# Performance work log

Measured on AMD Instinct MI355X. Metric: run time of the kernel, lower is better.

The kernel has to match this reference:

```python
import jax, jax.numpy as jnp
import numpy as np

EDGES = np.array([[0,6],[0,5],[6,8],[5,7],[0,62],[62,63],[63,64],[59,64],[59,60],[60,61],[61,62],[0,74],[71,72],[72,73],[73,74],[74,75],[75,76],[76,77],[77,78],[78,79],[79,80],[80,81],[81,82],[71,82],[71,83],[77,87],[83,84],[84,85],[85,86],[86,87],[87,88],[88,89],[89,90],[83,90],[0,65],[65,66],[66,67],[67,68],[68,69],[69,70],[65,70],[7,91],[91,92],[92,93],[93,94],[94,95],[91,96],[96,97],[97,98],[98,99],[91,100],[100,101],[101,102],[102,103],[91,104],[104,105],[105,106],[106,107],[91,108],[108,109],[109,110],[110,111],[8,112],[112,113],[113,114],[114,115],[115,116],[112,117],[117,118],[118,119],[119,120],[112,121],[121,122],[122,123],[123,124],[112,125],[125,126],[126,127],[127,128],[112,129],[129,130],[130,131],[131,132]], dtype=np.int32)
N_NODES = 102


def _gcn_structure():
    # Keep only edges whose endpoints fit in the 102-node feature view,
    # add self-loops, and compute symmetric GCN normalization (PyG gcn_norm).
    keep = (EDGES[:, 0] < N_NODES) & (EDGES[:, 1] < N_NODES)
    e = EDGES[keep]
    row, col = e[:, 0], e[:, 1]
    loops = np.arange(N_NODES, dtype=np.int32)
    row_f = np.concatenate([row, loops])
    col_f = np.concatenate([col, loops])
    deg = np.zeros(N_NODES, dtype=np.float32)
    np.add.at(deg, col_f, 1.0)  # in-degree incl. self-loop
    dinv = 1.0 / np.sqrt(np.maximum(deg, 1.0))
    norm = (dinv[row_f] * dinv[col_f]).astype(np.float32)
    return row_f, col_f, norm

_ROW, _COL, _NORM = _gcn_structure()


def setup_inputs() -> dict:
    key = jax.random.key(0)
    ks = jax.random.split(key, 5)
    B = 8192
    return {
        "x": jax.random.normal(ks[0], (B, 204), dtype=jnp.float32),
        "W_gcn": jax.random.normal(ks[1], (2, 64), dtype=jnp.float32) * 0.5,
        "b_gcn": jax.random.normal(ks[2], (64,), dtype=jnp.float32) * 0.1,
        "W_proj": jax.random.normal(ks[3], (64, 128), dtype=jnp.float32) * 0.1,
        "b_proj": jax.random.normal(ks[4], (128,), dtype=jnp.float32) * 0.1,
    }


def reference(x, W_gcn, b_gcn, W_proj, b_proj):
    B = x.shape[0]
    xn = x.reshape(B, N_NODES, 2)                      # (B, 102, 2)
    h = jnp.einsum('bni,ih->bnh', xn, W_gcn)           # GCN linear: (B, 102, H)
    norm = jnp.asarray(_NORM)
    msgs = h[:, _ROW, :] * norm[None, :, None]         # gather + normalize: (B, E+N, H)
    agg = jnp.zeros_like(h).at[:, _COL, :].add(msgs)   # scatter-add into targets
    agg = agg + b_gcn                                  # GCN bias
    act = jax.nn.relu(agg)                             # activation
    out = jnp.einsum('bnh,he->bne', act, W_proj) + b_proj  # projection: (B, 102, 128)
    return out
```

## Files before the change

### kernel.cpp

```cpp
#include <hip/hip_runtime.h>
#include <hip/hip_bf16.h>

#define NN   102
#define NE   83
#define NPAD 128

using bf16x8 = __attribute__((ext_vector_type(8))) short;
using f32x4  = __attribute__((ext_vector_type(4))) float;

__device__ __constant__ int EDGES_C[NE * 2] = {
    0,6, 0,5, 6,8, 5,7, 0,62, 62,63, 63,64, 59,64, 59,60, 60,61, 61,62,
    0,74, 71,72, 72,73, 73,74, 74,75, 75,76, 76,77, 77,78, 78,79, 79,80,
    80,81, 81,82, 71,82, 71,83, 77,87, 83,84, 84,85, 85,86, 86,87, 87,88,
    88,89, 89,90, 83,90, 0,65, 65,66, 66,67, 67,68, 68,69, 69,70, 65,70,
    7,91, 91,92, 92,93, 93,94, 94,95, 91,96, 96,97, 97,98, 98,99, 91,100,
    100,101, 101,102, 102,103, 91,104, 104,105, 105,106, 106,107, 91,108,
    108,109, 109,110, 110,111, 8,112, 112,113, 113,114, 114,115, 115,116,
    112,117, 117,118, 118,119, 119,120, 112,121, 121,122, 122,123, 123,124,
    112,125, 125,126, 126,127, 127,128, 112,129, 129,130, 130,131, 131,132
};

#define WS_BFRAG 0
#define WS_OFF   16384
#define WS_ER    (16384 + 512)
#define WS_EN    (16384 + 512 + 1024)

__device__ inline unsigned short f2bf(float f) {
  union { float f; unsigned u; } v; v.f = f;
  unsigned r = v.u + 0x7fffu + ((v.u >> 16) & 1u);
  return (unsigned short)(r >> 16);
}

__device__ inline unsigned cvt_pk_bf16(float lo, float hi) {
  unsigned r;
  asm("v_cvt_pk_bf16_f32 %0, %1, %2" : "=v"(r) : "v"(lo), "v"(hi));
  return r;
}

__global__ void gnn_setup(const float* __restrict__ Wp, char* __restrict__ ws) {
  const int t = threadIdx.x;

  if (blockIdx.x != 0) {
    unsigned short* bf = (unsigned short*)(ws + WS_BFRAG);
    for (int idx = t; idx < 16 * 64; idx += 256) {
      int lane = idx & 63;
      int f    = idx >> 6;
      int mt   = f >> 1, kc = f & 1;
      int e    = mt * 16 + (lane & 15);
      int kb   = kc * 32 + (lane >> 4) * 8;
      unsigned short* dst = bf + idx * 8;
#pragma unroll
      for (int i = 0; i < 8; ++i) dst[i] = f2bf(Wp[(kb + i) * 128 + e]);
    }
    return;
  }

  __shared__ float s_dinv[NN];
  __shared__ int   s_cnt[NN];
  __shared__ int   s_off[NN + 1];

  if (t < NN) {
    int deg = 1, cnt = 1;
    for (int e = 0; e < NE; ++e) {
      int r = EDGES_C[2*e], c = EDGES_C[2*e+1];
      if (r < NN && c == t) { ++deg; ++cnt; }
    }
    s_dinv[t] = 1.0f / sqrtf((float)deg);
    s_cnt[t]  = cnt;
  }
  __syncthreads();
  if (t < NN) {
    int o = 0;
    for (int c = 0; c < t; ++c) o += s_cnt[c];
    s_off[t] = o;
    if (t == NN - 1) s_off[NN] = o + s_cnt[t];
  }
  __syncthreads();
  int*   off = (int*)(ws + WS_OFF);
  int*   er  = (int*)(ws + WS_ER);
  float* en  = (float*)(ws + WS_EN);
  if (t < NN) {
    int c = t, pos = s_off[c];
    float dc = s_dinv[c];
    er[pos] = c; en[pos] = dc * dc; ++pos;
    for (int e = 0; e < NE; ++e) {
      int r = EDGES_C[2*e], cc = EDGES_C[2*e+1];
      if (r < NN && cc == c) { er[pos] = r; en[pos] = s_dinv[r] * dc; ++pos; }
    }
    off[c] = s_off[c];
    if (c == 0) off[NN] = s_off[NN];
  }
}

__global__ __launch_bounds__(256, 4) void gnn_main(
    const float* __restrict__ x, const float* __restrict__ Wg,
    const float* __restrict__ bg, const float* __restrict__ bp,
    const char* __restrict__ ws, float* __restrict__ out, int B) {
  const int t    = threadIdx.x;
  const int lane = t & 63;
  const int wv   = t >> 6;
  const int b    = blockIdx.x * 4 + wv;

  __shared__ float  swg[128];
  __shared__ float  sbg[64];
  __shared__ float  sbp[128];
  __shared__ bf16x8 sfrag[1024];
  __shared__ float  sxw[4][208];
  __shared__ float  syw[4][NPAD][2];
  __shared__ float  st[4][16][68];

  if (t < 128) { swg[t] = Wg[t]; sbp[t] = bp[t]; }
  if (t < 64)  sbg[t] = bg[t];
  {
    const f32x4* src = (const f32x4*)(ws + WS_BFRAG);
    f32x4* dst = (f32x4*)sfrag;
#pragma unroll
    for (int i = 0; i < 4; ++i)
      dst[t + i * 256] = src[t + i * 256];
  }
  __syncthreads();

  if (b >= B) return;

  float* sx = sxw[wv];
  float (*sy)[2] = syw[wv];

  if (lane < 51)
    *(f32x4*)&sx[lane * 4] = *(const f32x4*)(x + (size_t)b * 204 + lane * 4);

  {
    const int*   off = (const int*)(ws + WS_OFF);
    const int*   er  = (const int*)(ws + WS_ER);
    const float* en  = (const float*)(ws + WS_EN);
#pragma unroll
    for (int half = 0; half < 2; ++half) {
      const int n = lane + half * 64;
      float y0 = 0.f, y1 = 0.f;
      if (n < NN) {
        int s = off[n], e2 = off[n + 1];
        for (int j = s; j < e2; ++j) {
          int r = er[j]; float w = en[j];
          y0 = fmaf(w, sx[2 * r],     y0);
          y1 = fmaf(w, sx[2 * r + 1], y1);
        }
      }
      sy[n][0] = y0; sy[n][1] = y1;
    }
  }

  const int l15 = lane & 15;
  const int lhi = lane >> 4;
  const int kb  = lhi * 8;
  const int rb  = lhi * 4;

  const f32x4 bph0 = *(const f32x4*)&sbp[l15 * 4];
  const f32x4 bph1 = *(const f32x4*)&sbp[64 + l15 * 4];

  float* ob = out + (size_t)b * (NN * 128);

  for (int nt = 0; nt < 7; ++nt) {
    const int node = nt * 16 + l15;
    const float y0 = sy[node][0], y1 = sy[node][1];
    bf16x8 Bact[2];
#pragma unroll
    for (int kc = 0; kc < 2; ++kc) {
      float v[8];
#pragma unroll
      for (int i = 0; i < 8; ++i) {
        int h = kc * 32 + kb + i;
        float a = fmaf(y0, swg[h], fmaf(y1, swg[64 + h], sbg[h]));
        v[i] = fmaxf(a, 0.f);
      }
      union { unsigned u[4]; bf16x8 f; } pk;
      pk.u[0] = cvt_pk_bf16(v[0], v[1]);
      pk.u[1] = cvt_pk_bf16(v[2], v[3]);
      pk.u[2] = cvt_pk_bf16(v[4], v[5]);
      pk.u[3] = cvt_pk_bf16(v[6], v[7]);
      Bact[kc] = pk.f;
    }

    const int rows = (nt < 6) ? 16 : (NN - 96);

#pragma unroll
    for (int h = 0; h < 2; ++h) {
      bf16x8 F[4][2];
#pragma unroll
      for (int m = 0; m < 4; ++m) {
        F[m][0] = sfrag[((h * 4 + m) * 2 + 0) * 64 + lane];
        F[m][1] = sfrag[((h * 4 + m) * 2 + 1) * 64 + lane];
      }
#pragma unroll
      for (int m = 0; m < 4; ++m) {
        f32x4 a = {0.f, 0.f, 0.f, 0.f};
        a = __builtin_amdgcn_mfma_f32_16x16x32_bf16(F[m][0], Bact[0], a, 0, 0, 0);
        a = __builtin_amdgcn_mfma_f32_16x16x32_bf16(F[m][1], Bact[1], a, 0, 0, 0);
        *(f32x4*)&st[wv][l15][m * 16 + rb] = a;
      }
#pragma unroll
      for (int pass = 0; pass < 4; ++pass) {
        const int n2 = pass * 4 + lhi;
        if (n2 < rows) {
          f32x4 row = *(const f32x4*)&st[wv][n2][l15 * 4];
          row = row + (h ? bph1 : bph0);
          __builtin_nontemporal_store(row,
              (f32x4*)(ob + (nt * 16 + n2) * 128 + h * 64 + l15 * 4));
        }
      }
    }
  }
}

extern "C" void kernel_launch(void* const* d_in, const int* in_sizes, int n_in,
                              void* d_out, int out_size, void* d_ws, size_t ws_size,
                              hipStream_t stream) {
  const float* x  = (const float*)d_in[0];
  const float* Wg = (const float*)d_in[1];
  const float* bg = (const float*)d_in[2];
  const float* Wp = (const float*)d_in[3];
  const float* bp = (const float*)d_in[4];
  float* out = (float*)d_out;
  const int B = in_sizes[0] / 204;

  gnn_setup<<<2, 256, 0, stream>>>(Wp, (char*)d_ws);
  gnn_main<<<(B + 3) / 4, 256, 0, stream>>>(x, Wg, bg, bp, (const char*)d_ws, out, B);
}
```

Before: 104.0 us.

## Make waves persistent over 4 samples with double-buffered aggregation and full-width stores

Each wave now loops over several batch samples (a grid a quarter the size), prefetching the next sample's x while computing the current one and computing its aggregation into a second buffer. CSR structure is staged in LDS instead of global memory. The MFMA output is stored as full 128-column rows from a wider staging tile. This amortizes per-block setup (copying the weight fragments into LDS) across several samples and aims to improve store coalescing, but it lowers block count and raises LDS use per block, which may reduce occupancy.

```diff
diff --git a/kernel.cpp b/kernel.cpp
--- a/kernel.cpp
+++ b/kernel.cpp
@@ -95,22 +95,30 @@
 __global__ __launch_bounds__(256, 4) void gnn_main(
     const float* __restrict__ x, const float* __restrict__ Wg,
     const float* __restrict__ bg, const float* __restrict__ bp,
-    const char* __restrict__ ws, float* __restrict__ out, int B) {
+    const char* __restrict__ ws, float* __restrict__ out, int B, int nwaves) {
   const int t    = threadIdx.x;
   const int lane = t & 63;
   const int wv   = t >> 6;
-  const int b    = blockIdx.x * 4 + wv;
+  const int wgid = blockIdx.x * 4 + wv;
 
   __shared__ float  swg[128];
   __shared__ float  sbg[64];
   __shared__ float  sbp[128];
   __shared__ bf16x8 sfrag[1024];
+  __shared__ int    soff[NN + 2];
+  __shared__ int    ser[256];
+  __shared__ float  sen[256];
   __shared__ float  sxw[4][208];
-  __shared__ float  syw[4][NPAD][2];
-  __shared__ float  st[4][16][68];
+  __shared__ float  syw[4][2][NPAD][2];
+  __shared__ float  st[4][16][132];
 
   if (t < 128) { swg[t] = Wg[t]; sbp[t] = bp[t]; }
   if (t < 64)  sbg[t] = bg[t];
+  if (t < NN + 1) soff[t] = ((const int*)(ws + WS_OFF))[t];
+  if (t < 256) {
+    ser[t] = ((const int*)(ws + WS_ER))[t];
+    sen[t] = ((const float*)(ws + WS_EN))[t];
+  }
   {
     const f32x4* src = (const f32x4*)(ws + WS_BFRAG);
     f32x4* dst = (f32x4*)sfrag;
@@ -120,93 +128,94 @@
   }
   __syncthreads();
 
-  if (b >= B) return;
+  const int l15 = lane & 15;
+  const int lhi = lane >> 4;
+  const int kb  = lhi * 8;
+  const int rb  = lhi * 4;
+  const int c32 = (lane & 31) * 4;
+  const int rhi = lane >> 5;
+
+  const f32x4 bpv = *(const f32x4*)&sbp[c32];
 
   float* sx = sxw[wv];
-  float (*sy)[2] = syw[wv];
-
-  if (lane < 51)
-    *(f32x4*)&sx[lane * 4] = *(const f32x4*)(x + (size_t)b * 204 + lane * 4);
-
-  {
-    const int*   off = (const int*)(ws + WS_OFF);
-    const int*   er  = (const int*)(ws + WS_ER);
-    const float* en  = (const float*)(ws + WS_EN);
+
+  auto load_x = [&](int b) {
+    if (lane < 51)
+      *(f32x4*)&sx[lane * 4] = *(const f32x4*)(x + (size_t)b * 204 + lane * 4);
+  };
+  auto comp_y = [&](int p) {
+    float (*sy)[2] = syw[wv][p];
 #pragma unroll
     for (int half = 0; half < 2; ++half) {
       const int n = lane + half * 64;
       float y0 = 0.f, y1 = 0.f;
       if (n < NN) {
-        int s = off[n], e2 = off[n + 1];
+        int s = soff[n], e2 = soff[n + 1];
         for (int j = s; j < e2; ++j) {
-          int r = er[j]; float w = en[j];
+          int r = ser[j]; float w = sen[j];
           y0 = fmaf(w, sx[2 * r],     y0);
           y1 = fmaf(w, sx[2 * r + 1], y1);
         }
       }
       sy[n][0] = y0; sy[n][1] = y1;
     }
-  }
-
-  const int l15 = lane & 15;
-  const int lhi = lane >> 4;
-  const int kb  = lhi * 8;
-  const int rb  = lhi * 4;
-
-  const f32x4 bph0 = *(const f32x4*)&sbp[l15 * 4];
-  const f32x4 bph1 = *(const f32x4*)&sbp[64 + l15 * 4];
-
-  float* ob = out + (size_t)b * (NN * 128);
-
-  for (int nt = 0; nt < 7; ++nt) {
-    const int node = nt * 16 + l15;
-    const float y0 = sy[node][0], y1 = sy[node][1];
-    bf16x8 Bact[2];
-#pragma unroll
-    for (int kc = 0; kc < 2; ++kc) {
-      float v[8];
-#pragma unroll
-      for (int i = 0; i < 8; ++i) {
-        int h = kc * 32 + kb + i;
-        float a = fmaf(y0, swg[h], fmaf(y1, swg[64 + h], sbg[h]));
-        v[i] = fmaxf(a, 0.f);
-      }
-      union { unsigned u[4]; bf16x8 f; } pk;
-      pk.u[0] = cvt_pk_bf16(v[0], v[1]);
-      pk.u[1] = cvt_pk_bf16(v[2], v[3]);
-      pk.u[2] = cvt_pk_bf16(v[4], v[5]);
-      pk.u[3] = cvt_pk_bf16(v[6], v[7]);
-      Bact[kc] = pk.f;
-    }
-
-    const int rows = (nt < 6) ? 16 : (NN - 96);
-
-#pragma unroll
-    for (int h = 0; h < 2; ++h) {
-      bf16x8 F[4][2];
-#pragma unroll
-      for (int m = 0; m < 4; ++m) {
-        F[m][0] = sfrag[((h * 4 + m) * 2 + 0) * 64 + lane];
-        F[m][1] = sfrag[((h * 4 + m) * 2 + 1) * 64 + lane];
-      }
-#pragma unroll
-      for (int m = 0; m < 4; ++m) {
+  };
+
+  if (wgid < B) { load_x(wgid); comp_y(0); }
+
+  int i = 0;
+  for (int b = wgid; b < B; b += nwaves, ++i) {
+    const int p  = i & 1;
+    const int bn = b + nwaves;
+    if (bn < B) load_x(bn);
+    float (*sy)[2] = syw[wv][p];
+    float* ob = out + (size_t)b * (NN * 128);
+
+    for (int nt = 0; nt < 7; ++nt) {
+      const int node = nt * 16 + l15;
+      const float y0 = sy[node][0], y1 = sy[node][1];
+      bf16x8 Bact[2];
+#pragma unroll
+      for (int kc = 0; kc < 2; ++kc) {
+        float v[8];
+#pragma unroll
+        for (int ii = 0; ii < 8; ++ii) {
+          int h = kc * 32 + kb + ii;
+          float a = fmaf(y0, swg[h], fmaf(y1, swg[64 + h], sbg[h]));
+          v[ii] = fmaxf(a, 0.f);
+        }
+        union { unsigned u[4]; bf16x8 f; } pk;
+        pk.u[0] = cvt_pk_bf16(v[0], v[1]);
+        pk.u[1] = cvt_pk_bf16(v[2], v[3]);
+        pk.u[2] = cvt_pk_bf16(v[4], v[5]);
+        pk.u[3] = cvt_pk_bf16(v[6], v[7]);
+        Bact[kc] = pk.f;
+      }
+
+#pragma unroll
+      for (int m = 0; m < 8; ++m) {
+        bf16x8 F0 = sfrag[(m * 2 + 0) * 64 + lane];
+        bf16x8 F1 = sfrag[(m * 2 + 1) * 64 + lane];
         f32x4 a = {0.f, 0.f, 0.f, 0.f};
-        a = __builtin_amdgcn_mfma_f32_16x16x32_bf16(F[m][0], Bact[0], a, 0, 0, 0);
-        a = __builtin_amdgcn_mfma_f32_16x16x32_bf16(F[m][1], Bact[1], a, 0, 0, 0);
+        a = __builtin_amdgcn_mfma_f32_16x16x32_bf16(F0, Bact[0], a, 0, 0, 0);
+        a = __builtin_amdgcn_mfma_f32_16x16x32_bf16(F1, Bact[1], a, 0, 0, 0);
         *(f32x4*)&st[wv][l15][m * 16 + rb] = a;
       }
-#pragma unroll
-      for (int pass = 0; pass < 4; ++pass) {
-        const int n2 = pass * 4 + lhi;
+
+      const int rows = (nt < 6) ? 16 : (NN - 96);
+#pragma unroll
+      for (int pass = 0; pass < 8; ++pass) {
+        const int n2 = pass * 2 + rhi;
         if (n2 < rows) {
-          f32x4 row = *(const f32x4*)&st[wv][n2][l15 * 4];
-          row = row + (h ? bph1 : bph0);
+          f32x4 row = *(const f32x4*)&st[wv][n2][c32];
+          row = row + bpv;
           __builtin_nontemporal_store(row,
-              (f32x4*)(ob + (nt * 16 + n2) * 128 + h * 64 + l15 * 4));
+              (f32x4*)(ob + (nt * 16 + n2) * 128 + c32));
         }
       }
     }
+
+    if (bn < B) comp_y(p ^ 1);
   }
 }
 
@@ -221,6 +230,9 @@
   float* out = (float*)d_out;
   const int B = in_sizes[0] / 204;
 
+  const int grid = (B + 15) / 16;
+  const int nwaves = grid * 4;
+
   gnn_setup<<<2, 256, 0, stream>>>(Wp, (char*)d_ws);
-  gnn_main<<<(B + 3) / 4, 256, 0, stream>>>(x, Wg, bg, bp, (const char*)d_ws, out, B);
-}
+  gnn_main<<<grid, 256, 0, stream>>>(x, Wg, bg, bp, (const char*)d_ws, out, B, nwaves);
+}
```

Result: no change. 103.5 us (-0.4%).
